# Kernel optimization log

Measured on AMD Instinct MI355X. Metric: run time of the kernel, lower is better.

Reference implementation:

```python
import jax, jax.numpy as jnp
import numpy as np

N = 50000          # nodes
E = 1_600_000      # edges
R = 16             # num_relations
NB = 4             # num_bases
FIN = 128          # num_node_features
H = 128            # hidden_channels
G = 64             # num graphs in batch
NC = 2             # num_classes


def rgcn_conv(x, edge_index, edge_type, bases, comp, root, bias):
    """PyG RGCNConv with basis decomposition, mean aggregation per relation."""
    n = x.shape[0]
    # weight[r] = sum_b comp[r,b] * bases[b]  -> [R, in, out]
    weight = jnp.einsum('rb,bio->rio', comp, bases)
    src, dst = edge_index[0], edge_index[1]
    # segment id combining destination node and relation
    seg = dst * R + edge_type                      # [E]
    msg = x[src]                                   # [E, in] gather
    summed = jax.ops.segment_sum(msg, seg, num_segments=n * R)      # [N*R, in]
    cnt = jax.ops.segment_sum(jnp.ones((msg.shape[0],), x.dtype), seg,
                              num_segments=n * R)                   # [N*R]
    mean = summed / jnp.maximum(cnt, 1.0)[:, None]
    mean = mean.reshape(n, R, -1)                  # [N, R, in]
    out = jnp.einsum('nri,rio->no', mean, weight) + x @ root + bias
    return out


def global_mean_pool(x, batch, num_graphs):
    s = jax.ops.segment_sum(x, batch, num_segments=num_graphs)
    c = jax.ops.segment_sum(jnp.ones((x.shape[0],), x.dtype), batch,
                            num_segments=num_graphs)
    return s / jnp.maximum(c, 1.0)[:, None]


def setup_inputs() -> dict:
    key = jax.random.key(0)
    ks = jax.random.split(key, 24)
    inp = {
        'x': jax.random.normal(ks[0], (N, FIN), jnp.float32),
        'edge_index': jax.random.randint(ks[1], (2, E), 0, N),
        'edge_type': jax.random.randint(ks[2], (E,), 0, R),
        'batch': jnp.sort(jax.random.randint(ks[3], (N,), 0, G)),
        'rel_labels': jax.random.randint(ks[4], (G,), 0, R),
        'drop_prob': 0,
        'rel_emb': jax.random.normal(ks[5], (R, H), jnp.float32),
    }
    s1 = 1.0 / np.sqrt(FIN)
    s2 = 1.0 / np.sqrt(H)
    inp['bases1'] = jax.random.normal(ks[6], (NB, FIN, H), jnp.float32) * s1
    inp['comp1'] = jax.random.normal(ks[7], (R, NB), jnp.float32)
    inp['root1'] = jax.random.normal(ks[8], (FIN, H), jnp.float32) * s1
    inp['bias1'] = jnp.zeros((H,), jnp.float32)
    inp['bases2'] = jax.random.normal(ks[9], (NB, H, H), jnp.float32) * s2
    inp['comp2'] = jax.random.normal(ks[10], (R, NB), jnp.float32)
    inp['root2'] = jax.random.normal(ks[11], (H, H), jnp.float32) * s2
    inp['bias2'] = jnp.zeros((H,), jnp.float32)
    inp['bases3'] = jax.random.normal(ks[12], (NB, H, H), jnp.float32) * s2
    inp['comp3'] = jax.random.normal(ks[13], (R, NB), jnp.float32)
    inp['root3'] = jax.random.normal(ks[14], (H, H), jnp.float32) * s2
    inp['bias3'] = jnp.zeros((H,), jnp.float32)
    inp['lin_w'] = jax.random.normal(ks[15], (2 * H, NC), jnp.float32) * (1.0 / np.sqrt(2 * H))
    inp['lin_b'] = jnp.zeros((NC,), jnp.float32)
    return inp


def reference(x, edge_index, edge_type, batch, rel_labels, drop_prob, rel_emb,
              bases1, comp1, root1, bias1,
              bases2, comp2, root2, bias2,
              bases3, comp3, root3, bias3,
              lin_w, lin_b):
    rel_embs = rel_emb[rel_labels]                               # [G, H]
    h = jax.nn.relu(rgcn_conv(x, edge_index, edge_type, bases1, comp1, root1, bias1))
    h = jax.nn.relu(rgcn_conv(h, edge_index, edge_type, bases2, comp2, root2, bias2))
    h = rgcn_conv(h, edge_index, edge_type, bases3, comp3, root3, bias3)
    pooled = global_mean_pool(h, batch, G)                       # [G, H]
    z = jnp.concatenate([pooled, rel_embs], axis=1)              # [G, 2H]
    # dropout with p=drop_prob in eval mode (reference is deterministic) -> identity
    return z @ lin_w + lin_b                                     # [G, NC]
```

## Files before the change

kernel.cpp:

```cpp
#include <hip/hip_runtime.h>

#define NN 50000
#define EE 1600000
#define RR 16
#define NBASE 4
#define FINF 128
#define HD 128
#define NG 64
#define NCLS 2
#define NRSEG (NN*RR)

typedef __attribute__((ext_vector_type(8))) short short8;
typedef __attribute__((ext_vector_type(4))) float f32x4;
typedef __attribute__((ext_vector_type(2))) float f32x2;
typedef unsigned short u16;
typedef unsigned int u32;
typedef unsigned long long u64;
typedef unsigned char u8;

__device__ __forceinline__ float bflo(u32 u){ return __builtin_bit_cast(float, u << 16); }
__device__ __forceinline__ float bfhi(u32 u){ return __builtin_bit_cast(float, u & 0xFFFF0000u); }
__device__ __forceinline__ u16 f2bf(float f){
  u32 u = __builtin_bit_cast(u32, f);
  u += 0x7FFFu + ((u >> 16) & 1u);
  return (u16)(u >> 16);
}
__device__ __forceinline__ u32 pack2(float a, float b){
  return (u32)f2bf(a) | ((u32)f2bf(b) << 16);
}
__device__ __forceinline__ float ldf(const void* p, int i, int isbf){
  return isbf ? bflo((u32)((const u16*)p)[i]) : ((const float*)p)[i];
}

__device__ __forceinline__ float fp8_manual(u32 b){
  u32 s = (b>>7)&1, e = (b>>3)&15, m = b&7;
  float v;
  if (e==0) v = (float)m * 0.001953125f;
  else      v = __builtin_bit_cast(float, ((e+120u)<<23) | (m<<20));
  return s ? -v : v;
}
__device__ __forceinline__ u32 f32_to_fp8_manual(float f){
  u32 u = __builtin_bit_cast(u32, f);
  u32 s = u>>31;
  int e = (int)((u>>23)&0xFF);
  u32 m = u & 0x7FFFFF;
  int ee = e - 120;
  if (ee <= 0) return s<<7;
  u32 m3 = m >> 20, rem = m & 0xFFFFF;
  u32 rnd = (rem > 0x80000u) || (rem == 0x80000u && (m3 & 1));
  m3 += rnd;
  if (m3 == 8){ m3 = 0; ee += 1; }
  if (ee >= 16){ ee = 15; m3 = 6; }
  return (s<<7) | ((u32)ee<<3) | m3;
}
__device__ __forceinline__ void fp8x2_to_f32(u32 v, float& a, float& b){
#if __has_builtin(__builtin_amdgcn_cvt_pk_f32_fp8)
  f32x2 r = __builtin_amdgcn_cvt_pk_f32_fp8((int)v, false);
  a = r[0]; b = r[1];
#else
  a = fp8_manual(v & 0xFF); b = fp8_manual((v>>8)&0xFF);
#endif
}
__device__ __forceinline__ u32 pk_fp8x2(float a, float b){
  a = fminf(fmaxf(a, -448.f), 448.f);
  b = fminf(fmaxf(b, -448.f), 448.f);
#if __has_builtin(__builtin_amdgcn_cvt_pk_fp8_f32)
  return (u32)__builtin_amdgcn_cvt_pk_fp8_f32(a, b, 0, false) & 0xFFFF;
#else
  return f32_to_fp8_manual(a) | (f32_to_fp8_manual(b) << 8);
#endif
}

__global__ void k_detect(const u32* __restrict__ xw, int* __restrict__ flag){
  __shared__ int votes;
  if (threadIdx.x == 0) votes = 0;
  __syncthreads();
  u32 w = xw[threadIdx.x];
  int e = (w >> 7) & 0xFF;
  if (e >= 100 && e <= 129) atomicAdd(&votes, 1);
  __syncthreads();
  if (threadIdx.x == 0) flag[0] = (votes >= 192) ? 1 : 0;
}

__global__ void k_quant(const void* __restrict__ src, u8* __restrict__ dstq,
                        const int* __restrict__ flagp){
  int i = blockIdx.x*256 + threadIdx.x;
  if (i >= NN*HD/4) return;
  int isbf = flagp[0];
  float v0,v1,v2,v3;
  if (isbf){
    u32 a = ((const u32*)src)[i*2+0], b = ((const u32*)src)[i*2+1];
    v0=bflo(a); v1=bfhi(a); v2=bflo(b); v3=bfhi(b);
  } else {
    float4 f = ((const float4*)src)[i];
    v0=f.x; v1=f.y; v2=f.z; v3=f.w;
  }
  u32 q = pk_fp8x2(v0,v1) | (pk_fp8x2(v2,v3) << 16);
  ((u32*)dstq)[i] = q;
}


__global__ void k_hist(const int* __restrict__ dst, const int* __restrict__ et,
                       int* __restrict__ cnt){
  int e = blockIdx.x*256 + threadIdx.x;
  if (e < EE) atomicAdd(&cnt[et[e]*NN + dst[e]], 1);
}

__global__ void k_scan1(const int* __restrict__ cnt, int* __restrict__ off,
                        int* __restrict__ bsum){
  __shared__ int sh[256];
  int tid = threadIdx.x;
  int i = blockIdx.x*256 + tid;
  int v = (i < NRSEG) ? cnt[i] : 0;
  sh[tid] = v; __syncthreads();
  for (int d=1; d<256; d<<=1){
    int t = (tid >= d) ? sh[tid-d] : 0;
    __syncthreads();
    sh[tid] += t;
    __syncthreads();
  }
  if (i < NRSEG) off[i] = sh[tid] - v;
  if (tid == 255) bsum[blockIdx.x] = sh[255];
}

__global__ __launch_bounds__(1024) void k_scan2(int* __restrict__ bsum, int nb){
  __shared__ int sh[1024];
  __shared__ int carry;
  int tid = threadIdx.x;
  if (tid == 0) carry = 0;
  __syncthreads();
  for (int base=0; base<nb; base+=1024){
    int i = base + tid;
    int v = (i < nb) ? bsum[i] : 0;
    int orig = v;
    sh[tid] = v; __syncthreads();
    for (int d=1; d<1024; d<<=1){
      int t = (tid >= d) ? sh[tid-d] : 0;
      __syncthreads();
      sh[tid] += t;
      __syncthreads();
    }
    int total = sh[1023];
    int excl = sh[tid] - orig + carry;
    if (i < nb) bsum[i] = excl;
    __syncthreads();
    if (tid == 0) carry += total;
    __syncthreads();
  }
}

__global__ void k_scan3(const int* __restrict__ cnt, int* __restrict__ off,
                        const int* __restrict__ bsum){
  int i = blockIdx.x*256 + threadIdx.x;
  if (i < NRSEG){
    int o = off[i] + bsum[blockIdx.x];
    off[i] = o;
    if (i == NRSEG-1) off[NRSEG] = o + cnt[i];
  }
}

__global__ void k_scatter(const int* __restrict__ src, const int* __restrict__ dst,
                          const int* __restrict__ et, const int* __restrict__ off,
                          int* __restrict__ cnt, int* __restrict__ esrc){
  int e = blockIdx.x*256 + threadIdx.x;
  if (e < EE){
    int seg = et[e]*NN + dst[e];
    int p = atomicSub(&cnt[seg], 1) - 1;
    esrc[off[seg] + p] = src[e];
  }
}


__global__ void k_weights(const void* __restrict__ bases, const void* __restrict__ comp,
                          const void* __restrict__ root, u16* __restrict__ WTf,
                          const int* __restrict__ flagp){
  int idx = blockIdx.x*256 + threadIdx.x;
  if (idx >= 17*16384) return;
  int isbf = flagp[0];
  int r = idx >> 14;
  int o = (idx >> 7) & 127;
  int i = idx & 127;
  float v;
  if (r < RR){
    v = 0.f;
    #pragma unroll
    for (int b=0;b<NBASE;b++)
      v += ldf(comp, r*NBASE+b, isbf) * ldf(bases, (b*FINF + i)*HD + o, isbf);
  } else {
    v = ldf(root, i*HD + o, isbf);
  }
  int wv = o >> 5, ct = (o >> 4) & 1, mrow = o & 15;
  int ks = i >> 5, quad = (i >> 3) & 3, j = i & 7;
  int lane = quad*16 + mrow;
  WTf[(u32)((((r*4+wv)*2+ct)*4+ks)*64 + lane)*8 + j] = f2bf(v);
}


#define TN 16
#define ECAP 128

__global__ __launch_bounds__(256) void k_layer(
    const u8*  __restrict__ xq,
    const u16* __restrict__ WTf,
    const void* __restrict__ bias, const int* __restrict__ off,
    const int* __restrict__ esrc,
    u16* __restrict__ hout,
    u8* __restrict__ hq,
    const int* __restrict__ flagp, int write_bf, int relu)
{
  __shared__ __align__(16) u16 Abuf[4][TN*136];
  __shared__ int soff[RR*17];
  __shared__ int sesrc[4][ECAP];
  int tid = threadIdx.x;
  int n0 = blockIdx.x * TN;
  int isbf_in = flagp[0];

  int wv = tid >> 6;
  int lane = tid & 63;
  int mrow = lane & 15;
  int quad = lane >> 4;

  for (int i = tid; i < RR*17; i += 256){
    int r = i / 17, k = i - r*17;
    soff[i] = off[r*NN + n0 + k];
  }
  __syncthreads();

  f32x4 acc[2];
  { f32x4 z = {0.f,0.f,0.f,0.f}; acc[0] = z; acc[1] = z; }

  for (int t=0; t<4; ++t){
    int r = t*4 + wv;
    {
      int offv = 0;
      if (lane <= 16) offv = soff[r*17 + lane];
      int wstart = __builtin_amdgcn_readlane(offv, 0);
      int wend   = __builtin_amdgcn_readlane(offv, 16);
      int blen = wend - wstart;
      bool staged = (blen <= ECAP);
      if (staged){
        for (int j = lane; j < blen; j += 64) sesrc[wv][j] = esrc[wstart + j];
      }
      float a0 = 0.f, a1 = 0.f;
      int idx = 0;
      int cb  = wstart;
      int nb  = __builtin_amdgcn_readlane(offv, 1);
      u16* abase = Abuf[wv] + lane*2;

      auto flushTo = [&](int elim){
        while (idx < TN && nb <= elim){
          int cnt = nb - cb;
          float inv = (cnt > 0) ? (1.0f/(float)cnt) : 0.0f;
          *(u32*)(abase + idx*136) = pack2(a0*inv, a1*inv);
          a0 = 0.f; a1 = 0.f;
          cb = nb; idx++;
          if (idx < TN) nb = __builtin_amdgcn_readlane(offv, idx+1);
        }
      };

      if (staged){
        const int* sp = sesrc[wv];
        for (int e0i = wstart; e0i < wend; e0i += 16){
          int s8[16];
          #pragma unroll
          for (int j=0;j<16;j++){
            int ee = e0i + j;
            int ec = ee < wend ? ee : (wend - 1);
            s8[j] = sp[ec - wstart];
          }
          u32 w8[16];
          #pragma unroll
          for (int j=0;j<16;j++)
            w8[j] = (u32)(*(const u16*)(xq + (u32)s8[j]*HD + (u32)lane*2));
          #pragma unroll
          for (int j=0;j<16;j++){
            int ee = e0i + j;
            if (ee < wend){
              flushTo(ee);
              float da, db; fp8x2_to_f32(w8[j], da, db);
              a0 += da; a1 += db;
            }
          }
        }
      } else {
        for (int e0i = wstart; e0i < wend; e0i += 16){
          int s8[16];
          #pragma unroll
          for (int j=0;j<16;j++){
            int ee = e0i + j;
            int ec = ee < wend ? ee : (wend - 1);
            s8[j] = esrc[ec];
          }
          u32 w8[16];
          #pragma unroll
          for (int j=0;j<16;j++)
            w8[j] = (u32)(*(const u16*)(xq + (u32)s8[j]*HD + (u32)lane*2));
          #pragma unroll
          for (int j=0;j<16;j++){
            int ee = e0i + j;
            if (ee < wend){
              flushTo(ee);
              float da, db; fp8x2_to_f32(w8[j], da, db);
              a0 += da; a1 += db;
            }
          }
        }
      }
      flushTo(0x7fffffff);
    }
    __syncthreads();
    #pragma unroll
    for (int rloc=0; rloc<4; ++rloc){
      int rr = t*4 + rloc;
      const u16* Bp = WTf + (u32)(((rr*4 + wv)*2)*4*64)*8 + (u32)lane*8;
      #pragma unroll
      for (int ks=0; ks<4; ++ks){
        short8 af = *(const short8*)(Abuf[rloc] + mrow*136 + ks*32 + quad*8);
        #pragma unroll
        for (int ct=0; ct<2; ++ct){
          short8 bf = *(const short8*)(Bp + (u32)(ct*4 + ks)*64*8);
          acc[ct] = __builtin_amdgcn_mfma_f32_16x16x32_bf16(af, bf, acc[ct], 0, 0, 0);
        }
      }
    }
    __syncthreads();
  }
  {
    const u8* xrow = xq + (u32)(n0 + mrow)*HD;
    const u16* Bp = WTf + (u32)(((16*4 + wv)*2)*4*64)*8 + (u32)lane*8;
    #pragma unroll
    for (int ks=0; ks<4; ++ks){
      u32 lo = *(const u32*)(xrow + ks*32 + quad*8);
      u32 hi = *(const u32*)(xrow + ks*32 + quad*8 + 4);
      float f0,f1,f2,f3,f4,f5,f6,f7;
      fp8x2_to_f32(lo & 0xFFFFu, f0, f1);
      fp8x2_to_f32(lo >> 16,     f2, f3);
      fp8x2_to_f32(hi & 0xFFFFu, f4, f5);
      fp8x2_to_f32(hi >> 16,     f6, f7);
      union { short8 v; u32 w[4]; } u;
      u.w[0] = pack2(f0,f1); u.w[1] = pack2(f2,f3);
      u.w[2] = pack2(f4,f5); u.w[3] = pack2(f6,f7);
      #pragma unroll
      for (int ct=0; ct<2; ++ct){
        short8 bf = *(const short8*)(Bp + (u32)(ct*4 + ks)*64*8);
        acc[ct] = __builtin_amdgcn_mfma_f32_16x16x32_bf16(u.v, bf, acc[ct], 0, 0, 0);
      }
    }
  }
  #pragma unroll
  for (int ct=0; ct<2; ++ct){
    int col = wv*32 + ct*16 + mrow;
    float bv = ldf(bias, col, isbf_in);
    #pragma unroll
    for (int rg=0; rg<4; ++rg){
      int n = n0 + quad*4 + rg;
      float v = acc[ct][rg] + bv;
      if (relu) v = fmaxf(v, 0.f);
      if (!(v == v)) v = 0.f;
      if (write_bf) hout[(u32)(n*HD + col)] = f2bf(v);
      else          hq[(u32)(n*HD + col)] = (u8)(pk_fp8x2(v, 0.f) & 0xFF);
    }
  }
}


__global__ __launch_bounds__(1024) void k_pool_head(
    const u16* __restrict__ h, const int* __restrict__ batch,
    const int* __restrict__ rlab, const void* __restrict__ rel_emb,
    const void* __restrict__ lin_w, const void* __restrict__ lin_b,
    void* __restrict__ out, const int* __restrict__ flagp)
{
  int g = blockIdx.x;
  int isbf = flagp[0];
  __shared__ int bounds[2];
  __shared__ float psum[8][128];
  __shared__ float red[4];
  if (threadIdx.x == 0){
    int lo=0, hi=NN;
    while (lo < hi){ int m=(lo+hi)>>1; if (batch[m] < g) lo=m+1; else hi=m; }
    bounds[0] = lo;
    int lo2=lo, hi2=NN;
    while (lo2 < hi2){ int m=(lo2+hi2)>>1; if (batch[m] < g+1) lo2=m+1; else hi2=m; }
    bounds[1] = lo2;
  }
  __syncthreads();
  int lo = bounds[0], hi = bounds[1];
  int f = threadIdx.x & 127;
  int s = threadIdx.x >> 7;
  float acc = 0.f;
  for (int n = lo + s; n < hi; n += 8) acc += bflo((u32)h[(u32)(n*HD + f)]);
  psum[s][f] = acc;
  __syncthreads();
  if (threadIdx.x < 128){
    int cn = hi - lo;
    float tot = 0.f;
    #pragma unroll
    for (int k=0;k<8;k++) tot += psum[k][f];
    float pooled = tot / (float)(cn > 0 ? cn : 1);
    int rl = rlab[g];
    float re = ldf(rel_emb, rl*HD + f, isbf);
    float v0 = pooled * ldf(lin_w, f*NCLS+0, isbf) + re * ldf(lin_w, (HD+f)*NCLS+0, isbf);
    float v1 = pooled * ldf(lin_w, f*NCLS+1, isbf) + re * ldf(lin_w, (HD+f)*NCLS+1, isbf);
    #pragma unroll
    for (int o=32;o>0;o>>=1){ v0 += __shfl_down(v0,o); v1 += __shfl_down(v1,o); }
    int ln = threadIdx.x & 63, wvv = threadIdx.x >> 6;
    if (ln == 0){ red[wvv*2] = v0; red[wvv*2+1] = v1; }
  }
  __syncthreads();
  if (threadIdx.x == 0){
    float o0 = red[0] + red[2] + ldf(lin_b, 0, isbf);
    float o1 = red[1] + red[3] + ldf(lin_b, 1, isbf);
    if (isbf){
      ((u16*)out)[g*NCLS+0] = f2bf(o0);
      ((u16*)out)[g*NCLS+1] = f2bf(o1);
    } else {
      ((float*)out)[g*NCLS+0] = o0;
      ((float*)out)[g*NCLS+1] = o1;
    }
  }
}


extern "C" void kernel_launch(void* const* d_in, const int* in_sizes, int n_in,
                              void* d_out, int out_size, void* d_ws, size_t ws_size,
                              hipStream_t stream)
{
  (void)in_sizes; (void)n_in; (void)out_size; (void)ws_size;
  const void* x      = d_in[0];
  const int* eidx    = (const int*)d_in[1];
  const int* etype   = (const int*)d_in[2];
  const int* batch   = (const int*)d_in[3];
  const int* rlab    = (const int*)d_in[4];
  const void* rel_emb = d_in[6];
  const void* basesA[3] = {d_in[7],  d_in[11], d_in[15]};
  const void* compA[3]  = {d_in[8],  d_in[12], d_in[16]};
  const void* rootA[3]  = {d_in[9],  d_in[13], d_in[17]};
  const void* biasA[3]  = {d_in[10], d_in[14], d_in[18]};
  const void* lin_w  = d_in[19];
  const void* lin_b  = d_in[20];

  char* p = (char*)d_ws;
  auto alloc = [&](size_t bytes)->char*{ char* r = p; p += (bytes + 255) & ~(size_t)255; return r; };
  int*   flag   = (int*)  alloc(256);
  int*   off    = (int*)  alloc((size_t)(NRSEG+1)*4);
  int*   esrc   = (int*)  alloc((size_t)(EE+64)*4);
  u16*   WTf    = (u16*)  alloc((size_t)17*16384*2);
  u8*    xq     = (u8*)   alloc((size_t)NN*HD);
  u8*    h1q    = (u8*)   alloc((size_t)NN*HD);
  u8*    h2q    = (u8*)   alloc((size_t)NN*HD);
  u16*   h3     = (u16*)  alloc((size_t)NN*HD*2);
  int*   cnt    = (int*)h3;
  int*   bsum   = (int*)((char*)h3 + (size_t)NRSEG*4);

  const int* src_in = eidx;
  const int* dst_in = eidx + EE;

  k_detect <<<1, 256, 0, stream>>>((const u32*)x, flag);
  hipMemsetAsync(cnt, 0, (size_t)NRSEG*4, stream);
  k_quant  <<<(NN*HD/4 + 255)/256, 256, 0, stream>>>(x, xq, flag);
  k_hist   <<<EE/256,    256, 0, stream>>>(dst_in, etype, cnt);
  k_scan1  <<<NRSEG/256, 256, 0, stream>>>(cnt, off, bsum);
  k_scan2  <<<1,        1024, 0, stream>>>(bsum, NRSEG/256);
  k_scan3  <<<NRSEG/256, 256, 0, stream>>>(cnt, off, bsum);
  k_scatter<<<EE/256,    256, 0, stream>>>(src_in, dst_in, etype, off, cnt, esrc);

  const int nblk = NN / TN;
  k_weights<<<1088, 256, 0, stream>>>(basesA[0], compA[0], rootA[0], WTf, flag);
  k_layer<<<nblk, 256, 0, stream>>>(xq,  WTf, biasA[0], off, esrc, (u16*)0, h1q, flag, 0, 1);
  k_weights<<<1088, 256, 0, stream>>>(basesA[1], compA[1], rootA[1], WTf, flag);
  k_layer<<<nblk, 256, 0, stream>>>(h1q, WTf, biasA[1], off, esrc, (u16*)0, h2q, flag, 0, 1);
  k_weights<<<1088, 256, 0, stream>>>(basesA[2], compA[2], rootA[2], WTf, flag);
  k_layer<<<nblk, 256, 0, stream>>>(h2q, WTf, biasA[2], off, esrc, h3, (u8*)0, flag, 1, 0);

  k_pool_head<<<NG, 1024, 0, stream>>>(h3, batch, rlab, rel_emb, lin_w, lin_b,
                                       d_out, flag);
}
```

Before: 654.8 us.

## Restructure edge gather with register-prefetched sources, merge setup kernels, bigger scan blocks

```diff
diff --git a/kernel.cpp b/kernel.cpp
--- a/kernel.cpp
+++ b/kernel.cpp
@@ -27,6 +27,18 @@
 }
 __device__ __forceinline__ u32 pack2(float a, float b){
   return (u32)f2bf(a) | ((u32)f2bf(b) << 16);
+}
+__device__ __forceinline__ u32 cvt_pk_bf16(float a, float b){
+  u32 r;
+  asm("v_cvt_pk_bf16_f32 %0, %1, %2" : "=v"(r) : "v"(a), "v"(b));
+  return r;
+}
+__device__ __forceinline__ float fastrcp(float x){
+#if __has_builtin(__builtin_amdgcn_rcpf)
+  return __builtin_amdgcn_rcpf(x);
+#else
+  return 1.0f / x;
+#endif
 }
 __device__ __forceinline__ float ldf(const void* p, int i, int isbf){
   return isbf ? bflo((u32)((const u16*)p)[i]) : ((const float*)p)[i];
@@ -83,8 +95,9 @@
 }
 
 __global__ void k_quant(const void* __restrict__ src, u8* __restrict__ dstq,
-                        const int* __restrict__ flagp){
+                        const int* __restrict__ flagp, int* __restrict__ cnt){
   int i = blockIdx.x*256 + threadIdx.x;
+  if (i < NRSEG) cnt[i] = 0;
   if (i >= NN*HD/4) return;
   int isbf = flagp[0];
   float v0,v1,v2,v3;
@@ -106,21 +119,23 @@
   if (e < EE) atomicAdd(&cnt[et[e]*NN + dst[e]], 1);
 }
 
-__global__ void k_scan1(const int* __restrict__ cnt, int* __restrict__ off,
-                        int* __restrict__ bsum){
-  __shared__ int sh[256];
+#define SCB 1024
+__global__ __launch_bounds__(SCB) void k_scan1(const int* __restrict__ cnt,
+                                               int* __restrict__ off,
+                                               int* __restrict__ bsum){
+  __shared__ int sh[SCB];
   int tid = threadIdx.x;
-  int i = blockIdx.x*256 + tid;
+  int i = blockIdx.x*SCB + tid;
   int v = (i < NRSEG) ? cnt[i] : 0;
   sh[tid] = v; __syncthreads();
-  for (int d=1; d<256; d<<=1){
+  for (int d=1; d<SCB; d<<=1){
     int t = (tid >= d) ? sh[tid-d] : 0;
     __syncthreads();
     sh[tid] += t;
     __syncthreads();
   }
   if (i < NRSEG) off[i] = sh[tid] - v;
-  if (tid == 255) bsum[blockIdx.x] = sh[255];
+  if (tid == SCB-1) bsum[blockIdx.x] = sh[SCB-1];
 }
 
 __global__ __launch_bounds__(1024) void k_scan2(int* __restrict__ bsum, int nb){
@@ -149,9 +164,10 @@
   }
 }
 
-__global__ void k_scan3(const int* __restrict__ cnt, int* __restrict__ off,
-                        const int* __restrict__ bsum){
-  int i = blockIdx.x*256 + threadIdx.x;
+__global__ __launch_bounds__(SCB) void k_scan3(const int* __restrict__ cnt,
+                                               int* __restrict__ off,
+                                               const int* __restrict__ bsum){
+  int i = blockIdx.x*SCB + threadIdx.x;
   if (i < NRSEG){
     int o = off[i] + bsum[blockIdx.x];
     off[i] = o;
@@ -171,11 +187,22 @@
 }
 
 
-__global__ void k_weights(const void* __restrict__ bases, const void* __restrict__ comp,
-                          const void* __restrict__ root, u16* __restrict__ WTf,
-                          const int* __restrict__ flagp){
-  int idx = blockIdx.x*256 + threadIdx.x;
+__global__ void k_weights3(const void* __restrict__ b0, const void* __restrict__ c0,
+                           const void* __restrict__ r0,
+                           const void* __restrict__ b1, const void* __restrict__ c1,
+                           const void* __restrict__ r1,
+                           const void* __restrict__ b2, const void* __restrict__ c2,
+                           const void* __restrict__ r2,
+                           u16* __restrict__ WTf, const int* __restrict__ flagp){
+  int gid = blockIdx.x;
+  int layer = gid / 1088;
+  int blk = gid - layer*1088;
+  int idx = blk*256 + threadIdx.x;
   if (idx >= 17*16384) return;
+  const void* bases = (layer==0) ? b0 : (layer==1) ? b1 : b2;
+  const void* comp  = (layer==0) ? c0 : (layer==1) ? c1 : c2;
+  const void* root  = (layer==0) ? r0 : (layer==1) ? r1 : r2;
+  u16* W = WTf + (u32)layer * (17*16384);
   int isbf = flagp[0];
   int r = idx >> 14;
   int o = (idx >> 7) & 127;
@@ -192,14 +219,13 @@
   int wv = o >> 5, ct = (o >> 4) & 1, mrow = o & 15;
   int ks = i >> 5, quad = (i >> 3) & 3, j = i & 7;
   int lane = quad*16 + mrow;
-  WTf[(u32)((((r*4+wv)*2+ct)*4+ks)*64 + lane)*8 + j] = f2bf(v);
+  W[(u32)((((r*4+wv)*2+ct)*4+ks)*64 + lane)*8 + j] = f2bf(v);
 }
 
 
 #define TN 16
-#define ECAP 128
-
-__global__ __launch_bounds__(256) void k_layer(
+
+__global__ __launch_bounds__(256, 6) void k_layer(
     const u8*  __restrict__ xq,
     const u16* __restrict__ WTf,
     const void* __restrict__ bias, const int* __restrict__ off,
@@ -210,13 +236,13 @@
 {
   __shared__ __align__(16) u16 Abuf[4][TN*136];
   __shared__ int soff[RR*17];
-  __shared__ int sesrc[4][ECAP];
   int tid = threadIdx.x;
   int n0 = blockIdx.x * TN;
   int isbf_in = flagp[0];
 
   int wv = tid >> 6;
   int lane = tid & 63;
+  int lane2 = lane << 1;
   int mrow = lane & 15;
   int quad = lane >> 4;
 
@@ -237,76 +263,79 @@
       int wstart = __builtin_amdgcn_readlane(offv, 0);
       int wend   = __builtin_amdgcn_readlane(offv, 16);
       int blen = wend - wstart;
-      bool staged = (blen <= ECAP);
-      if (staged){
-        for (int j = lane; j < blen; j += 64) sesrc[wv][j] = esrc[wstart + j];
-      }
+
       float a0 = 0.f, a1 = 0.f;
       int idx = 0;
-      int cb  = wstart;
-      int nb  = __builtin_amdgcn_readlane(offv, 1);
+      int cb = wstart;
+      int nb = __builtin_amdgcn_readlane(offv, 1);
       u16* abase = Abuf[wv] + lane*2;
 
-      auto flushTo = [&](int elim){
-        while (idx < TN && nb <= elim){
-          int cnt = nb - cb;
-          float inv = (cnt > 0) ? (1.0f/(float)cnt) : 0.0f;
-          *(u32*)(abase + idx*136) = pack2(a0*inv, a1*inv);
-          a0 = 0.f; a1 = 0.f;
-          cb = nb; idx++;
-          if (idx < TN) nb = __builtin_amdgcn_readlane(offv, idx+1);
-        }
+      auto doflush = [&](){
+        int cnt = nb - cb;
+        float cf = (float)(cnt > 0 ? cnt : 1);
+        float inv = fastrcp(cf);
+        *(u32*)(abase + idx*136) = cvt_pk_bf16(a0*inv, a1*inv);
+        a0 = 0.f; a1 = 0.f;
+        cb = nb; idx++;
+        if (idx < TN) nb = __builtin_amdgcn_readlane(offv, idx+1);
       };
-
-      if (staged){
-        const int* sp = sesrc[wv];
-        for (int e0i = wstart; e0i < wend; e0i += 16){
-          int s8[16];
+      auto consume = [&](int ae, u32 w){
+        while (idx < TN && nb <= ae) doflush();
+        float da, db; fp8x2_to_f32(w, da, db);
+        a0 += da; a1 += db;
+      };
+
+      if (blen > 0 && blen <= 128){
+        int ei0 = esrc[wstart + (lane < blen ? lane : 0)];
+        int ei1 = (blen > 64) ? esrc[wstart + 64 + (lane < blen-64 ? lane : 0)] : 0;
+
+        auto section = [&](int eiv, int sbeg, int L){
+          u32 wa[8], wb[8];
           #pragma unroll
-          for (int j=0;j<16;j++){
-            int ee = e0i + j;
-            int ec = ee < wend ? ee : (wend - 1);
-            s8[j] = sp[ec - wstart];
+          for (int k=0;k<8;k++){
+            int ee = k < L ? k : L-1;
+            int sid = __builtin_amdgcn_readlane(eiv, ee);
+            wa[k] = (u32)*(const u16*)(xq + ((u64)(u32)sid << 7) + lane2);
           }
-          u32 w8[16];
-          #pragma unroll
-          for (int j=0;j<16;j++)
-            w8[j] = (u32)(*(const u16*)(xq + (u32)s8[j]*HD + (u32)lane*2));
-          #pragma unroll
-          for (int j=0;j<16;j++){
-            int ee = e0i + j;
-            if (ee < wend){
-              flushTo(ee);
-              float da, db; fp8x2_to_f32(w8[j], da, db);
-              a0 += da; a1 += db;
+          for (int b0 = 0; b0 < L; b0 += 16){
+            if (b0 + 8 < L){
+              #pragma unroll
+              for (int k=0;k<8;k++){
+                int e2 = b0+8+k; int ee = e2 < L ? e2 : L-1;
+                int sid = __builtin_amdgcn_readlane(eiv, ee);
+                wb[k] = (u32)*(const u16*)(xq + ((u64)(u32)sid << 7) + lane2);
+              }
+            }
+            #pragma unroll
+            for (int k=0;k<8;k++){
+              int e = b0 + k;
+              if (e < L) consume(sbeg + e, wa[k]);
+            }
+            if (b0 + 16 < L){
+              #pragma unroll
+              for (int k=0;k<8;k++){
+                int e2 = b0+16+k; int ee = e2 < L ? e2 : L-1;
+                int sid = __builtin_amdgcn_readlane(eiv, ee);
+                wa[k] = (u32)*(const u16*)(xq + ((u64)(u32)sid << 7) + lane2);
+              }
+            }
+            #pragma unroll
+            for (int k=0;k<8;k++){
+              int e = b0 + 8 + k;
+              if (e < L) consume(sbeg + e, wb[k]);
             }
           }
-        }
-      } else {
-        for (int e0i = wstart; e0i < wend; e0i += 16){
-          int s8[16];
-          #pragma unroll
-          for (int j=0;j<16;j++){
-            int ee = e0i + j;
-            int ec = ee < wend ? ee : (wend - 1);
-            s8[j] = esrc[ec];
-          }
-          u32 w8[16];
-          #pragma unroll
-          for (int j=0;j<16;j++)
-            w8[j] = (u32)(*(const u16*)(xq + (u32)s8[j]*HD + (u32)lane*2));
-          #pragma unroll
-          for (int j=0;j<16;j++){
-            int ee = e0i + j;
-            if (ee < wend){
-              flushTo(ee);
-              float da, db; fp8x2_to_f32(w8[j], da, db);
-              a0 += da; a1 += db;
-            }
-          }
+        };
+        int L0 = blen < 64 ? blen : 64;
+        section(ei0, wstart, L0);
+        if (blen > 64) section(ei1, wstart + 64, blen - 64);
+      } else if (blen > 0){
+        for (int e = wstart; e < wend; ++e){
+          int sid = __builtin_amdgcn_readfirstlane(esrc[e]);
+          consume(e, (u32)*(const u16*)(xq + ((u64)(u32)sid << 7) + lane2));
         }
       }
-      flushTo(0x7fffffff);
+      while (idx < TN) doflush();
     }
     __syncthreads();
     #pragma unroll
@@ -338,8 +367,8 @@
       fp8x2_to_f32(hi & 0xFFFFu, f4, f5);
       fp8x2_to_f32(hi >> 16,     f6, f7);
       union { short8 v; u32 w[4]; } u;
-      u.w[0] = pack2(f0,f1); u.w[1] = pack2(f2,f3);
-      u.w[2] = pack2(f4,f5); u.w[3] = pack2(f6,f7);
+      u.w[0] = cvt_pk_bf16(f0,f1); u.w[1] = cvt_pk_bf16(f2,f3);
+      u.w[2] = cvt_pk_bf16(f4,f5); u.w[3] = cvt_pk_bf16(f6,f7);
       #pragma unroll
       for (int ct=0; ct<2; ++ct){
         short8 bf = *(const short8*)(Bp + (u32)(ct*4 + ks)*64*8);
@@ -444,7 +473,7 @@
   int*   flag   = (int*)  alloc(256);
   int*   off    = (int*)  alloc((size_t)(NRSEG+1)*4);
   int*   esrc   = (int*)  alloc((size_t)(EE+64)*4);
-  u16*   WTf    = (u16*)  alloc((size_t)17*16384*2);
+  u16*   WTf    = (u16*)  alloc((size_t)3*17*16384*2);
   u8*    xq     = (u8*)   alloc((size_t)NN*HD);
   u8*    h1q    = (u8*)   alloc((size_t)NN*HD);
   u8*    h2q    = (u8*)   alloc((size_t)NN*HD);
@@ -455,22 +484,28 @@
   const int* src_in = eidx;
   const int* dst_in = eidx + EE;
 
+  const int nscan = (NRSEG + SCB - 1) / SCB;
+
   k_detect <<<1, 256, 0, stream>>>((const u32*)x, flag);
-  hipMemsetAsync(cnt, 0, (size_t)NRSEG*4, stream);
-  k_quant  <<<(NN*HD/4 + 255)/256, 256, 0, stream>>>(x, xq, flag);
-  k_hist   <<<EE/256,    256, 0, stream>>>(dst_in, etype, cnt);
-  k_scan1  <<<NRSEG/256, 256, 0, stream>>>(cnt, off, bsum);
-  k_scan2  <<<1,        1024, 0, stream>>>(bsum, NRSEG/256);
-  k_scan3  <<<NRSEG/256, 256, 0, stream>>>(cnt, off, bsum);
-  k_scatter<<<EE/256,    256, 0, stream>>>(src_in, dst_in, etype, off, cnt, esrc);
+  k_quant  <<<(NN*HD/4 + 255)/256, 256, 0, stream>>>(x, xq, flag, cnt);
+  k_hist   <<<EE/256, 256, 0, stream>>>(dst_in, etype, cnt);
+  k_scan1  <<<nscan, SCB, 0, stream>>>(cnt, off, bsum);
+  k_scan2  <<<1,    1024, 0, stream>>>(bsum, nscan);
+  k_scan3  <<<nscan, SCB, 0, stream>>>(cnt, off, bsum);
+  k_scatter<<<EE/256, 256, 0, stream>>>(src_in, dst_in, etype, off, cnt, esrc);
+
+  k_weights3<<<3*1088, 256, 0, stream>>>(basesA[0], compA[0], rootA[0],
+                                         basesA[1], compA[1], rootA[1],
+                                         basesA[2], compA[2], rootA[2],
+                                         WTf, flag);
 
   const int nblk = NN / TN;
-  k_weights<<<1088, 256, 0, stream>>>(basesA[0], compA[0], rootA[0], WTf, flag);
-  k_layer<<<nblk, 256, 0, stream>>>(xq,  WTf, biasA[0], off, esrc, (u16*)0, h1q, flag, 0, 1);
-  k_weights<<<1088, 256, 0, stream>>>(basesA[1], compA[1], rootA[1], WTf, flag);
-  k_layer<<<nblk, 256, 0, stream>>>(h1q, WTf, biasA[1], off, esrc, (u16*)0, h2q, flag, 0, 1);
-  k_weights<<<1088, 256, 0, stream>>>(basesA[2], compA[2], rootA[2], WTf, flag);
-  k_layer<<<nblk, 256, 0, stream>>>(h2q, WTf, biasA[2], off, esrc, h3, (u8*)0, flag, 1, 0);
+  u16* W0 = WTf;
+  u16* W1 = WTf + (size_t)1*17*16384;
+  u16* W2 = WTf + (size_t)2*17*16384;
+  k_layer<<<nblk, 256, 0, stream>>>(xq,  W0, biasA[0], off, esrc, (u16*)0, h1q, flag, 0, 1);
+  k_layer<<<nblk, 256, 0, stream>>>(h1q, W1, biasA[1], off, esrc, (u16*)0, h2q, flag, 0, 1);
+  k_layer<<<nblk, 256, 0, stream>>>(h2q, W2, biasA[2], off, esrc, h3, (u8*)0, flag, 1, 0);
 
   k_pool_head<<<NG, 1024, 0, stream>>>(h3, batch, rlab, rel_emb, lin_w, lin_b,
                                        d_out, flag);
```

Measured after the change: 643.3 us. No clear change (-1.7%).
